# Kernel tuning notes

Hardware: AMD Instinct MI355X
Metric: run time of the kernel (lower is better)

Reference implementation:

```python
import jax, jax.numpy as jnp
import numpy as np

# Module constants (from init_kwargs)
IN_PLANES = 32
NUM_FILTERS = 4
MAX_H = 128
MAX_W = 128
REPARAM_FACTOR = 8
REPARAM_H = MAX_H * REPARAM_FACTOR  # 1024
REPARAM_W = MAX_W * REPARAM_FACTOR  # 1024
NORMALIZE = True
BATCH = 8


def _init_box_params(key):
    """Random valid boxes (mimics reset_parameters), returned in the
    reparametrized (scaled-down) form stored in the module."""
    k1, k2, k3, k4 = jax.random.split(key, 4)
    shape = (IN_PLANES, NUM_FILTERS)
    # actual box coordinates: x_min < 0 < x_max, comfortably inside the image
    x_min = jax.random.uniform(k1, shape, minval=-MAX_H / 3.0, maxval=-2.0)
    x_max = jax.random.uniform(k2, shape, minval=2.0, maxval=MAX_H / 3.0)
    y_min = jax.random.uniform(k3, shape, minval=-MAX_W / 3.0, maxval=-2.0)
    y_max = jax.random.uniform(k4, shape, minval=2.0, maxval=MAX_W / 3.0)
    # store in reparametrized form (divide by reparametrization scale)
    return (x_min / REPARAM_H, x_max / REPARAM_H,
            y_min / REPARAM_W, y_max / REPARAM_W)


def setup_inputs() -> dict:
    key = jax.random.key(0)
    k_in, k_box = jax.random.split(key)
    inp = jax.random.normal(k_in, (BATCH, IN_PLANES, MAX_H, MAX_W), dtype=jnp.float32)
    x_min, x_max, y_min, y_max = _init_box_params(k_box)
    return {"input": inp,
            "x_min": x_min.astype(jnp.float32), "x_max": x_max.astype(jnp.float32),
            "y_min": y_min.astype(jnp.float32), "y_max": y_max.astype(jnp.float32)}


def reference(input, x_min, x_max, y_min, y_max):
    B, C, H, W = input.shape
    F = x_min.shape[1]

    # undo reparametrization -> actual continuous box coordinates
    xmin = x_min * REPARAM_H
    xmax = x_max * REPARAM_H
    ymin = y_min * REPARAM_W
    ymax = y_max * REPARAM_W

    # integral image with a zero row/col on top/left: ii[b,c,i,j] = sum input[:i,:j]
    ii = jnp.pad(jnp.cumsum(jnp.cumsum(input, axis=2), axis=3),
                 ((0, 0), (0, 0), (1, 0), (1, 0)))  # [B,C,H+1,W+1]

    h_idx = jnp.arange(H, dtype=input.dtype)
    w_idx = jnp.arange(W, dtype=input.dtype)

    # continuous corner coordinates per (channel, filter, output position),
    # clipped into the valid integral-image domain (zero padding outside)
    xs_t = jnp.clip(h_idx[None, None, :] + xmin[:, :, None], 0.0, H)        # [C,F,H]
    xs_b = jnp.clip(h_idx[None, None, :] + xmax[:, :, None] + 1.0, 0.0, H)  # [C,F,H]
    ys_l = jnp.clip(w_idx[None, None, :] + ymin[:, :, None], 0.0, W)        # [C,F,W]
    ys_r = jnp.clip(w_idx[None, None, :] + ymax[:, :, None] + 1.0, 0.0, W)  # [C,F,W]

    c_idx = jnp.arange(C)[:, None, None]  # [C,1,1]

    def x_interp(xs):
        # linear interpolation of integral-image rows at continuous x coords
        x0f = jnp.clip(jnp.floor(xs), 0.0, H - 1.0)   # [C,F,H]
        fx = xs - x0f
        x0 = x0f.astype(jnp.int32)
        r0 = ii[:, c_idx, x0, :]       # [B,C,F,H,W+1]
        r1 = ii[:, c_idx, x0 + 1, :]   # [B,C,F,H,W+1]
        return (1.0 - fx)[None, :, :, :, None] * r0 + fx[None, :, :, :, None] * r1

    def y_interp(rows, ys):
        # linear interpolation along W of x-interpolated integral rows
        y0f = jnp.clip(jnp.floor(ys), 0.0, W - 1.0)   # [C,F,W]
        fy = ys - y0f
        y0 = y0f.astype(jnp.int32)[None, :, :, None, :]  # [1,C,F,1,W]
        tgt = rows.shape[:-1] + (W,)
        g0 = jnp.take_along_axis(rows, jnp.broadcast_to(y0, tgt), axis=-1)
        g1 = jnp.take_along_axis(rows, jnp.broadcast_to(y0 + 1, tgt), axis=-1)
        return (1.0 - fy)[None, :, :, None, :] * g0 + fy[None, :, :, None, :] * g1

    rows_t = x_interp(xs_t)  # top edge
    rows_b = x_interp(xs_b)  # bottom edge

    # inclusion-exclusion over the four bilinearly-sampled corners
    out = (y_interp(rows_b, ys_r) - y_interp(rows_b, ys_l)) \
        - (y_interp(rows_t, ys_r) - y_interp(rows_t, ys_l))   # [B,C,F,H,W]

    if NORMALIZE:
        area = (xmax - xmin + 1.0) * (ymax - ymin + 1.0)  # [C,F]
        out = out / area[None, :, :, None, None]

    return out.reshape(B, C * F, H, W)
```

## Files before the change

### kernel.cpp

```cpp
#include <hip/hip_runtime.h>

#define BATCH 8
#define CC 32
#define FF 4
#define HH 128
#define WW 128
#define STRIDE 129
#define RP 1024.0f
#define NTHREADS 1024
#define NWAVES 16
#define DEW 260
#define DEBASE 64

__global__ __launch_bounds__(NTHREADS) void boxconv_kernel(
    const float* __restrict__ in,
    const float* __restrict__ xmin_p,
    const float* __restrict__ xmax_p,
    const float* __restrict__ ymin_p,
    const float* __restrict__ ymax_p,
    float* __restrict__ out)
{
    __shared__ float ii[(HH + 1) * STRIDE];
    __shared__ float de[NWAVES * DEW];
    __shared__ float partial[8 * 128];

    const int plane = blockIdx.x;
    const int c = plane & (CC - 1);
    const int tid = threadIdx.x;
    const int wave = tid >> 6;
    const int lane = tid & 63;
    const float* inp = in + (size_t)plane * (HH * WW);

    for (int i4 = tid; i4 < (HH * WW) / 4; i4 += NTHREADS) {
        const float4 v = ((const float4*)inp)[i4];
        const int idx = i4 << 2;
        const int x = idx >> 7;
        const int y = idx & (WW - 1);
        float* dst = &ii[(x + 1) * STRIDE + (y + 1)];
        dst[0] = v.x; dst[1] = v.y; dst[2] = v.z; dst[3] = v.w;
    }
    if (tid <= HH) {
        ii[tid] = 0.0f;
        ii[tid * STRIDE] = 0.0f;
    }
    de[wave * DEW + lane] = 0.0f;
    __syncthreads();

    {
        const int row = tid & 127, seg = tid >> 7;
        float* p = &ii[(row + 1) * STRIDE + 1 + seg * 16];
        float v[16];
        float s = 0.0f;
        #pragma unroll
        for (int j = 0; j < 16; ++j) { s += p[j]; v[j] = s; }
        partial[seg * 128 + row] = s;
        __syncthreads();
        float off = 0.0f;
        for (int k = 0; k < seg; ++k) off += partial[k * 128 + row];
        #pragma unroll
        for (int j = 0; j < 16; ++j) p[j] = v[j] + off;
    }
    __syncthreads();

    {
        const int col = tid & 127, seg = tid >> 7;
        float* p = &ii[(seg * 16 + 1) * STRIDE + col + 1];
        float v[16];
        float s = 0.0f;
        #pragma unroll
        for (int j = 0; j < 16; ++j) { s += p[j * STRIDE]; v[j] = s; }
        partial[seg * 128 + col] = s;
        __syncthreads();
        float off = 0.0f;
        for (int k = 0; k < seg; ++k) off += partial[k * 128 + col];
        #pragma unroll
        for (int j = 0; j < 16; ++j) p[j * STRIDE] = v[j] + off;
    }
    __syncthreads();

    float* De = &de[wave * DEW];
    for (int f = 0; f < FF; ++f) {
        const int pidx = c * FF + f;
        const float xmn = xmin_p[pidx] * RP;
        const float xmx = xmax_p[pidx] * RP;
        const float ymn = ymin_p[pidx] * RP;
        const float ymx = ymax_p[pidx] * RP;
        const float inv_area = 1.0f / ((xmx - xmn + 1.0f) * (ymx - ymn + 1.0f));
        const float ktf = floorf(xmn);          const int kt = (int)ktf;  const float ft = xmn - ktf;
        const float kbf = floorf(xmx + 1.0f);   const int kb = (int)kbf;  const float fb = xmx + 1.0f - kbf;
        const float klf = floorf(ymn);          const int kl = (int)klf;  const float fl = ymn - klf;
        const float krf = floorf(ymx + 1.0f);   const int kr = (int)krf;  const float fr = ymx + 1.0f - krf;
        const float gl = 1.0f - fl, gr = 1.0f - fr;
        const float* DlBase = De + DEBASE + kl;
        const float* DrBase = De + DEBASE + kr;
        float* outf = out + ((size_t)plane * FF + f) * (HH * WW);

        for (int h = wave; h < HH; h += NWAVES) {
            int rt = h + kt;
            float gt = 1.0f - ft, ftw = ft;
            if (rt < 0) { rt = 0; gt = 0.0f; ftw = 0.0f; }
            int rb = h + kb;
            float gb = 1.0f - fb, fbw = fb;
            if (rb > 127) { rb = 127; gb = 0.0f; fbw = 1.0f; }

            const float* pt = &ii[rt * STRIDE + lane];
            const float* pb = &ii[rb * STRIDE + lane];
            const float t0 = gt * pt[0]  + ftw * pt[STRIDE];
            const float t1 = gt * pt[64] + ftw * pt[64 + STRIDE];
            const float b0 = gb * pb[0]  + fbw * pb[STRIDE];
            const float b1 = gb * pb[64] + fbw * pb[64 + STRIDE];
            const float t2 = gt * pt[128 - lane] + ftw * pt[128 - lane + STRIDE];
            const float b2 = gb * pb[128 - lane] + fbw * pb[128 - lane + STRIDE];
            const float d128 = b2 - t2;

            De[DEBASE + lane]        = b0 - t0;
            De[DEBASE + 64 + lane]   = b1 - t1;
            if (lane == 0) De[DEBASE + 128] = d128;
            De[DEBASE + 129 + lane]  = d128;

            const float l0a = DlBase[lane],      l0b = DlBase[lane + 1];
            const float l1a = DlBase[lane + 64], l1b = DlBase[lane + 65];
            const float r0a = DrBase[lane],      r0b = DrBase[lane + 1];
            const float r1a = DrBase[lane + 64], r1b = DrBase[lane + 65];
            const float o0 = (gr * r0a + fr * r0b - gl * l0a - fl * l0b) * inv_area;
            const float o1 = (gr * r1a + fr * r1b - gl * l1a - fl * l1b) * inv_area;
            float* outr = outf + h * WW + lane;
            outr[0]  = o0;
            outr[64] = o1;
        }
    }
}

extern "C" void kernel_launch(void* const* d_in, const int* in_sizes, int n_in,
                              void* d_out, int out_size, void* d_ws, size_t ws_size,
                              hipStream_t stream) {
    const float* inp    = (const float*)d_in[0];
    const float* x_min  = (const float*)d_in[1];
    const float* x_max  = (const float*)d_in[2];
    const float* y_min  = (const float*)d_in[3];
    const float* y_max  = (const float*)d_in[4];
    float* out = (float*)d_out;

    dim3 grid(BATCH * CC);
    dim3 block(NTHREADS);
    boxconv_kernel<<<grid, block, 0, stream>>>(inp, x_min, x_max, y_min, y_max, out);
}
```

Measured before the change: 97.22 us.

## Split filters across two blocks per plane and stream contiguous row chunks per wave

Launches twice as many blocks, each handling two of the four filters for a plane with 512 threads. Every block rebuilds the integral image, so that work is duplicated. Each wave now owns a contiguous chunk of 16 output rows and carries the previous integral-image row in registers, which halves the LDS reads for the vertical interpolation. Clamping is simplified to index clamping into the padded 129-row table. The goal is better occupancy and less LDS traffic, paid for with a redundant prefix-sum pass per plane.

```diff
diff --git a/kernel.cpp b/kernel.cpp
--- a/kernel.cpp
+++ b/kernel.cpp
@@ -7,10 +7,11 @@
 #define WW 128
 #define STRIDE 129
 #define RP 1024.0f
-#define NTHREADS 1024
-#define NWAVES 16
-#define DEW 260
-#define DEBASE 64
+#define NTHREADS 512
+#define NWAVES 8
+#define CH 16
+#define DEW 244
+#define DEBASE 48
 
 __global__ __launch_bounds__(NTHREADS) void boxconv_kernel(
     const float* __restrict__ in,
@@ -22,9 +23,11 @@
 {
     __shared__ float ii[(HH + 1) * STRIDE];
     __shared__ float de[NWAVES * DEW];
-    __shared__ float partial[8 * 128];
+    __shared__ float partial[4 * 128];
 
-    const int plane = blockIdx.x;
+    const int bid = blockIdx.x;
+    const int plane = bid & 255;
+    const int fpair = bid >> 8;
     const int c = plane & (CC - 1);
     const int tid = threadIdx.x;
     const int wave = tid >> 6;
@@ -43,43 +46,46 @@
         ii[tid] = 0.0f;
         ii[tid * STRIDE] = 0.0f;
     }
-    de[wave * DEW + lane] = 0.0f;
+    if (lane < DEBASE) de[wave * DEW + lane] = 0.0f;
     __syncthreads();
 
     {
         const int row = tid & 127, seg = tid >> 7;
-        float* p = &ii[(row + 1) * STRIDE + 1 + seg * 16];
-        float v[16];
+        float* p = &ii[(row + 1) * STRIDE + 1 + seg * 32];
+        float v[32];
         float s = 0.0f;
         #pragma unroll
-        for (int j = 0; j < 16; ++j) { s += p[j]; v[j] = s; }
+        for (int j = 0; j < 32; ++j) { s += p[j]; v[j] = s; }
         partial[seg * 128 + row] = s;
         __syncthreads();
         float off = 0.0f;
         for (int k = 0; k < seg; ++k) off += partial[k * 128 + row];
         #pragma unroll
-        for (int j = 0; j < 16; ++j) p[j] = v[j] + off;
+        for (int j = 0; j < 32; ++j) p[j] = v[j] + off;
     }
     __syncthreads();
 
     {
         const int col = tid & 127, seg = tid >> 7;
-        float* p = &ii[(seg * 16 + 1) * STRIDE + col + 1];
-        float v[16];
+        float* p = &ii[(seg * 32 + 1) * STRIDE + col + 1];
+        float v[32];
         float s = 0.0f;
         #pragma unroll
-        for (int j = 0; j < 16; ++j) { s += p[j * STRIDE]; v[j] = s; }
+        for (int j = 0; j < 32; ++j) { s += p[j * STRIDE]; v[j] = s; }
         partial[seg * 128 + col] = s;
         __syncthreads();
         float off = 0.0f;
         for (int k = 0; k < seg; ++k) off += partial[k * 128 + col];
         #pragma unroll
-        for (int j = 0; j < 16; ++j) p[j * STRIDE] = v[j] + off;
+        for (int j = 0; j < 32; ++j) p[j * STRIDE] = v[j] + off;
     }
     __syncthreads();
 
     float* De = &de[wave * DEW];
-    for (int f = 0; f < FF; ++f) {
+    const int h0 = wave * CH;
+
+    for (int ff = 0; ff < 2; ++ff) {
+        const int f = fpair * 2 + ff;
         const int pidx = c * FF + f;
         const float xmn = xmin_p[pidx] * RP;
         const float xmx = xmax_p[pidx] * RP;
@@ -90,33 +96,34 @@
         const float kbf = floorf(xmx + 1.0f);   const int kb = (int)kbf;  const float fb = xmx + 1.0f - kbf;
         const float klf = floorf(ymn);          const int kl = (int)klf;  const float fl = ymn - klf;
         const float krf = floorf(ymx + 1.0f);   const int kr = (int)krf;  const float fr = ymx + 1.0f - krf;
-        const float gl = 1.0f - fl, gr = 1.0f - fr;
+        const float gt = 1.0f - ft, gb = 1.0f - fb, gl = 1.0f - fl, gr = 1.0f - fr;
         const float* DlBase = De + DEBASE + kl;
         const float* DrBase = De + DEBASE + kr;
         float* outf = out + ((size_t)plane * FF + f) * (HH * WW);
 
-        for (int h = wave; h < HH; h += NWAVES) {
-            int rt = h + kt;
-            float gt = 1.0f - ft, ftw = ft;
-            if (rt < 0) { rt = 0; gt = 0.0f; ftw = 0.0f; }
-            int rb = h + kb;
-            float gb = 1.0f - fb, fbw = fb;
-            if (rb > 127) { rb = 127; gb = 0.0f; fbw = 1.0f; }
+        int xt = h0 + kt;
+        int xb = h0 + kb;
+        float tp0, tp1, tp2, bp0, bp1, bp2;
+        {
+            const float* p = &ii[min(max(xt, 0), 128) * STRIDE];
+            tp0 = p[lane]; tp1 = p[lane + 64]; tp2 = p[128];
+            const float* q = &ii[min(max(xb, 0), 128) * STRIDE];
+            bp0 = q[lane]; bp1 = q[lane + 64]; bp2 = q[128];
+        }
 
-            const float* pt = &ii[rt * STRIDE + lane];
-            const float* pb = &ii[rb * STRIDE + lane];
-            const float t0 = gt * pt[0]  + ftw * pt[STRIDE];
-            const float t1 = gt * pt[64] + ftw * pt[64 + STRIDE];
-            const float b0 = gb * pb[0]  + fbw * pb[STRIDE];
-            const float b1 = gb * pb[64] + fbw * pb[64 + STRIDE];
-            const float t2 = gt * pt[128 - lane] + ftw * pt[128 - lane + STRIDE];
-            const float b2 = gb * pb[128 - lane] + fbw * pb[128 - lane + STRIDE];
-            const float d128 = b2 - t2;
+        for (int j = 0; j < CH; ++j) {
+            const float* p = &ii[min(max(xt + j + 1, 0), 128) * STRIDE];
+            const float tc0 = p[lane], tc1 = p[lane + 64], tc2 = p[128];
+            const float* q = &ii[min(max(xb + j + 1, 0), 128) * STRIDE];
+            const float bc0 = q[lane], bc1 = q[lane + 64], bc2 = q[128];
 
-            De[DEBASE + lane]        = b0 - t0;
-            De[DEBASE + 64 + lane]   = b1 - t1;
-            if (lane == 0) De[DEBASE + 128] = d128;
-            De[DEBASE + 129 + lane]  = d128;
+            const float d0   = (gb * bp0 + fb * bc0) - (gt * tp0 + ft * tc0);
+            const float d1   = (gb * bp1 + fb * bc1) - (gt * tp1 + ft * tc1);
+            const float d128 = (gb * bp2 + fb * bc2) - (gt * tp2 + ft * tc2);
+
+            De[DEBASE + lane]        = d0;
+            De[DEBASE + 64 + lane]   = d1;
+            De[DEBASE + 128 + lane]  = d128;
 
             const float l0a = DlBase[lane],      l0b = DlBase[lane + 1];
             const float l1a = DlBase[lane + 64], l1b = DlBase[lane + 65];
@@ -124,9 +131,12 @@
             const float r1a = DrBase[lane + 64], r1b = DrBase[lane + 65];
             const float o0 = (gr * r0a + fr * r0b - gl * l0a - fl * l0b) * inv_area;
             const float o1 = (gr * r1a + fr * r1b - gl * l1a - fl * l1b) * inv_area;
-            float* outr = outf + h * WW + lane;
+            float* outr = outf + (h0 + j) * WW + lane;
             outr[0]  = o0;
             outr[64] = o1;
+
+            tp0 = tc0; tp1 = tc1; tp2 = tc2;
+            bp0 = bc0; bp1 = bc1; bp2 = bc2;
         }
     }
 }
@@ -141,7 +151,7 @@
     const float* y_max  = (const float*)d_in[4];
     float* out = (float*)d_out;
 
-    dim3 grid(BATCH * CC);
+    dim3 grid(2 * BATCH * CC);
     dim3 block(NTHREADS);
     boxconv_kernel<<<grid, block, 0, stream>>>(inp, x_min, x_max, y_min, y_max, out);
 }
```

After: 100.5 us. +3.4%, slower.

## Assign contiguous row chunks per wave, reuse integral rows, vectorize LDS and stores

Applied to the files above, without the earlier changes.

Each wave now processes 8 consecutive output rows instead of rows strided by 16. This lets it carry the previous integral-image row in registers, so each step loads only one new row for the top edge and one for the bottom. LDS reads/writes and global stores become float2 with two adjacent columns per lane, aligned by splitting box offsets into even bases plus a select. The integral-image stride changes to 130 for float2 alignment. Clamping now uses min/max into the zero row/last row instead of explicit boundary weight overrides, which relies on the padded layout for correctness.

```diff
diff --git a/kernel.cpp b/kernel.cpp
--- a/kernel.cpp
+++ b/kernel.cpp
@@ -5,12 +5,13 @@
 #define FF 4
 #define HH 128
 #define WW 128
-#define STRIDE 129
+#define STRIDE 130
 #define RP 1024.0f
 #define NTHREADS 1024
 #define NWAVES 16
-#define DEW 260
-#define DEBASE 64
+#define CH 8
+#define DEW 240
+#define DEBASE 48
 
 __global__ __launch_bounds__(NTHREADS) void boxconv_kernel(
     const float* __restrict__ in,
@@ -43,7 +44,7 @@
         ii[tid] = 0.0f;
         ii[tid * STRIDE] = 0.0f;
     }
-    de[wave * DEW + lane] = 0.0f;
+    if (lane < DEBASE) de[wave * DEW + lane] = 0.0f;
     __syncthreads();
 
     {
@@ -79,6 +80,8 @@
     __syncthreads();
 
     float* De = &de[wave * DEW];
+    const int h0 = wave * CH;
+
     for (int f = 0; f < FF; ++f) {
         const int pidx = c * FF + f;
         const float xmn = xmin_p[pidx] * RP;
@@ -90,43 +93,54 @@
         const float kbf = floorf(xmx + 1.0f);   const int kb = (int)kbf;  const float fb = xmx + 1.0f - kbf;
         const float klf = floorf(ymn);          const int kl = (int)klf;  const float fl = ymn - klf;
         const float krf = floorf(ymx + 1.0f);   const int kr = (int)krf;  const float fr = ymx + 1.0f - krf;
-        const float gl = 1.0f - fl, gr = 1.0f - fr;
-        const float* DlBase = De + DEBASE + kl;
-        const float* DrBase = De + DEBASE + kr;
+        const float gt = 1.0f - ft, gb = 1.0f - fb, gl = 1.0f - fl, gr = 1.0f - fr;
+        const int al = kl & ~1, dl = kl - al;
+        const int ar = kr & ~1, dr = kr - ar;
+        const float* Lp = &De[DEBASE + al + 2 * lane];
+        const float* Rp = &De[DEBASE + ar + 2 * lane];
         float* outf = out + ((size_t)plane * FF + f) * (HH * WW);
 
-        for (int h = wave; h < HH; h += NWAVES) {
-            int rt = h + kt;
-            float gt = 1.0f - ft, ftw = ft;
-            if (rt < 0) { rt = 0; gt = 0.0f; ftw = 0.0f; }
-            int rb = h + kb;
-            float gb = 1.0f - fb, fbw = fb;
-            if (rb > 127) { rb = 127; gb = 0.0f; fbw = 1.0f; }
+        const int xt = h0 + kt;
+        const int xb = h0 + kb;
+        const float* p0 = &ii[min(max(xt, 0), 128) * STRIDE];
+        const float* q0 = &ii[min(max(xb, 0), 128) * STRIDE];
+        float2 tp = *(const float2*)&p0[2 * lane];
+        float  tp2 = p0[128];
+        float2 bp = *(const float2*)&q0[2 * lane];
+        float  bp2 = q0[128];
 
-            const float* pt = &ii[rt * STRIDE + lane];
-            const float* pb = &ii[rb * STRIDE + lane];
-            const float t0 = gt * pt[0]  + ftw * pt[STRIDE];
-            const float t1 = gt * pt[64] + ftw * pt[64 + STRIDE];
-            const float b0 = gb * pb[0]  + fbw * pb[STRIDE];
-            const float b1 = gb * pb[64] + fbw * pb[64 + STRIDE];
-            const float t2 = gt * pt[128 - lane] + ftw * pt[128 - lane + STRIDE];
-            const float b2 = gb * pb[128 - lane] + fbw * pb[128 - lane + STRIDE];
-            const float d128 = b2 - t2;
+        #pragma unroll
+        for (int j = 0; j < CH; ++j) {
+            const float* p = &ii[min(max(xt + j + 1, 0), 128) * STRIDE];
+            const float* q = &ii[min(max(xb + j + 1, 0), 128) * STRIDE];
+            const float2 tc = *(const float2*)&p[2 * lane];
+            const float  tc2 = p[128];
+            const float2 bc = *(const float2*)&q[2 * lane];
+            const float  bc2 = q[128];
 
-            De[DEBASE + lane]        = b0 - t0;
-            De[DEBASE + 64 + lane]   = b1 - t1;
-            if (lane == 0) De[DEBASE + 128] = d128;
-            De[DEBASE + 129 + lane]  = d128;
+            const float d0   = (gb * bp.x + fb * bc.x) - (gt * tp.x + ft * tc.x);
+            const float d1   = (gb * bp.y + fb * bc.y) - (gt * tp.y + ft * tc.y);
+            const float d128 = (gb * bp2  + fb * bc2 ) - (gt * tp2  + ft * tc2 );
 
-            const float l0a = DlBase[lane],      l0b = DlBase[lane + 1];
-            const float l1a = DlBase[lane + 64], l1b = DlBase[lane + 65];
-            const float r0a = DrBase[lane],      r0b = DrBase[lane + 1];
-            const float r1a = DrBase[lane + 64], r1b = DrBase[lane + 65];
-            const float o0 = (gr * r0a + fr * r0b - gl * l0a - fl * l0b) * inv_area;
-            const float o1 = (gr * r1a + fr * r1b - gl * l1a - fl * l1b) * inv_area;
-            float* outr = outf + h * WW + lane;
-            outr[0]  = o0;
-            outr[64] = o1;
+            *(float2*)&De[DEBASE + 2 * lane] = make_float2(d0, d1);
+            De[DEBASE + 128 + lane] = d128;
+
+            const float2 vL0 = *(const float2*)(Lp);
+            const float2 vL1 = *(const float2*)(Lp + 2);
+            const float2 vR0 = *(const float2*)(Rp);
+            const float2 vR1 = *(const float2*)(Rp + 2);
+            const float La = dl ? vL0.y : vL0.x;
+            const float Lb = dl ? vL1.x : vL0.y;
+            const float Lc = dl ? vL1.y : vL1.x;
+            const float Ra = dr ? vR0.y : vR0.x;
+            const float Rb = dr ? vR1.x : vR0.y;
+            const float Rc = dr ? vR1.y : vR1.x;
+
+            const float o0 = (gr * Ra + fr * Rb - gl * La - fl * Lb) * inv_area;
+            const float o1 = (gr * Rb + fr * Rc - gl * Lb - fl * Lc) * inv_area;
+            *(float2*)&outf[(h0 + j) * WW + 2 * lane] = make_float2(o0, o1);
+
+            tp = tc; tp2 = tc2; bp = bc; bp2 = bc2;
         }
     }
 }
```

New measurement: 96.69 us. No clear change (-0.5%).
